# Kernel tuning notes

Measured on AMD Instinct MI355X. Metric: run time of the kernel, lower is better.

Reference implementation:

```python
import jax, jax.numpy as jnp
import numpy as np

B, N = 32, 4096
SA1 = (512, 0.2, 32)   # npoint, radius, nsample
SA2 = (128, 0.4, 64)
MLP1 = [3, 64, 64, 128]
MLP2 = [131, 128, 128, 256]   # 128 feats + 3 relative xyz
MLP3 = [259, 256, 512, 1024]  # 256 feats + 3 xyz (group_all)


def _mk_mlp(key, dims, prefix, d):
    for i in range(len(dims) - 1):
        key, k1 = jax.random.split(key)
        d[f"{prefix}_w{i}"] = jax.random.normal(k1, (dims[i], dims[i + 1]), jnp.float32) * (1.0 / np.sqrt(dims[i]))
        d[f"{prefix}_b{i}"] = jnp.zeros((dims[i + 1],), jnp.float32)
    return key


def setup_inputs() -> dict:
    key = jax.random.key(0)
    d = {}
    key, kx = jax.random.split(key)
    d["xyz"] = jax.random.uniform(kx, (B, N, 3), jnp.float32)  # normalized coords in [0,1)
    key = _mk_mlp(key, MLP1, "sa1", d)
    key = _mk_mlp(key, MLP2, "sa2", d)
    key = _mk_mlp(key, MLP3, "sa3", d)
    key, k1, k2 = jax.random.split(key, 3)
    d["cls_w"] = jax.random.normal(k1, (1024, 1), jnp.float32) * 0.03
    d["cls_b"] = jnp.zeros((1,), jnp.float32)
    d["reg_w"] = jax.random.normal(k2, (1024, 4), jnp.float32) * 0.03
    d["reg_b"] = jnp.zeros((4,), jnp.float32)
    return d


def fps(xyz, npoint):
    """Farthest point sampling. xyz: (B,N,3) -> idx (B,npoint) int32."""
    Bb, Nn, _ = xyz.shape

    def step(carry, _):
        dist, farthest = carry  # (B,N), (B,)
        centroid = jnp.take_along_axis(xyz, farthest[:, None, None], axis=1)  # (B,1,3)
        d = jnp.sum((xyz - centroid) ** 2, axis=-1)  # (B,N)
        dist = jnp.minimum(dist, d)
        nxt = jnp.argmax(dist, axis=-1).astype(jnp.int32)
        return (dist, nxt), farthest

    init = (jnp.full((Bb, Nn), 1e10, xyz.dtype), jnp.zeros((Bb,), jnp.int32))
    _, idx = jax.lax.scan(step, init, None, length=npoint)
    return idx.T  # (B,npoint)


def ball_query(radius, nsample, xyz, new_xyz):
    """xyz: (B,N,3), new_xyz: (B,S,3) -> idx (B,S,nsample) int32."""
    Bb, S, _ = new_xyz.shape
    Nn = xyz.shape[1]
    sqr = jnp.sum((new_xyz[:, :, None, :] - xyz[:, None, :, :]) ** 2, axis=-1)  # (B,S,N)
    idx = jnp.broadcast_to(jnp.arange(Nn, dtype=jnp.int32), (Bb, S, Nn))
    idx = jnp.where(sqr > radius * radius, Nn, idx)
    idx = jnp.sort(idx, axis=-1)[:, :, :nsample]
    first = idx[:, :, :1]
    return jnp.where(idx == Nn, first, idx)  # pad out-of-ball slots with first neighbor


def _sa(xyz, feats, npoint, radius, nsample, ws, bs):
    Bb = xyz.shape[0]
    cidx = fps(xyz, npoint)
    new_xyz = xyz[jnp.arange(Bb)[:, None], cidx]  # (B,S,3)
    gidx = ball_query(radius, nsample, xyz, new_xyz)  # (B,S,K)
    b3 = jnp.arange(Bb)[:, None, None]
    g = xyz[b3, gidx] - new_xyz[:, :, None, :]  # (B,S,K,3) relative coords
    if feats is not None:
        g = jnp.concatenate([g, feats[b3, gidx]], axis=-1)
    for w, b in zip(ws, bs):
        g = jax.nn.relu(g @ w + b)
    return new_xyz, jnp.max(g, axis=2)  # (B,S,C_out)


def _sa_all(xyz, feats, ws, bs):
    g = jnp.concatenate([xyz, feats], axis=-1)[:, None]  # (B,1,S,3+C)
    for w, b in zip(ws, bs):
        g = jax.nn.relu(g @ w + b)
    return jnp.max(g, axis=2)[:, 0]  # (B,C_out)


def reference(xyz, sa1_w0, sa1_b0, sa1_w1, sa1_b1, sa1_w2, sa1_b2,
              sa2_w0, sa2_b0, sa2_w1, sa2_b1, sa2_w2, sa2_b2,
              sa3_w0, sa3_b0, sa3_w1, sa3_b1, sa3_w2, sa3_b2,
              cls_w, cls_b, reg_w, reg_b):
    xyz1, f1 = _sa(xyz, None, SA1[0], SA1[1], SA1[2],
                   [sa1_w0, sa1_w1, sa1_w2], [sa1_b0, sa1_b1, sa1_b2])
    xyz2, f2 = _sa(xyz1, f1, SA2[0], SA2[1], SA2[2],
                   [sa2_w0, sa2_w1, sa2_w2], [sa2_b0, sa2_b1, sa2_b2])
    feat = _sa_all(xyz2, f2, [sa3_w0, sa3_w1, sa3_w2], [sa3_b0, sa3_b1, sa3_b2])  # (B,1024)
    return feat @ cls_w + cls_b, feat @ reg_w + reg_b
```

## Files before the change

kernel.cpp:

```cpp
#include <hip/hip_runtime.h>

#define DEVINL __device__ __forceinline__

typedef __attribute__((ext_vector_type(8))) short bf16x8;
typedef __attribute__((ext_vector_type(8))) unsigned short u16x8;
typedef __attribute__((ext_vector_type(4))) float f32x4;

DEVINL unsigned short f2bh(float f){
  unsigned u = __float_as_uint(f);
  return (unsigned short)((u + 0x7FFFu + ((u >> 16) & 1u)) >> 16);
}
DEVINL float bh2f(unsigned short h){ return __uint_as_float(((unsigned)h) << 16); }

DEVINL unsigned long long dpp_max_u64(unsigned long long k) {
#define DPP_STEP(ctrl)                                                        \
  {                                                                           \
    int hi = (int)(k >> 32), lo = (int)(unsigned)k;                           \
    int oh = __builtin_amdgcn_update_dpp(0, hi, ctrl, 0xF, 0xF, 1);           \
    int ol = __builtin_amdgcn_update_dpp(0, lo, ctrl, 0xF, 0xF, 1);           \
    unsigned long long ok =                                                   \
        ((unsigned long long)(unsigned)oh << 32) | (unsigned)ol;              \
    if (ok > k) k = ok;                                                       \
  }
  DPP_STEP(0x111)
  DPP_STEP(0x112)
  DPP_STEP(0x114)
  DPP_STEP(0x118)
  DPP_STEP(0x142)
  DPP_STEP(0x143)
#undef DPP_STEP
  return k;
}

template<int N, int NP, int NT>
DEVINL void fps_body(const float* __restrict__ xyz, float* __restrict__ nxyz,
                     int b, int t) {
  constexpr int PTS = N / NT;
  constexpr int NW = NT / 64;
  __shared__ float xs[N], ys[N], zs[N];
  __shared__ int farr[NP];
  __shared__ unsigned long long sk[2][(NW > 1 ? NW : 1)];
  float px[PTS], py[PTS], pz[PTS], dst[PTS];
  const float* base = xyz + (size_t)b * N * 3;
#pragma unroll
  for (int j = 0; j < PTS; ++j) {
    int i = t + j * NT;
    float x = base[i * 3 + 0], y = base[i * 3 + 1], z = base[i * 3 + 2];
    px[j] = x; py[j] = y; pz[j] = z;
    xs[i] = x; ys[i] = y; zs[i] = z;
    dst[j] = 1e10f;
  }
  __syncthreads();
  int far = 0;
  const int wv = t >> 6, ln = t & 63;
  for (int s = 0; s < NP; ++s) {
    float cx = xs[far], cy = ys[far], cz = zs[far];
    if (t == 0) farr[s] = far;
    float bv = -1.f; int bi = 0;
#pragma unroll
    for (int j = 0; j < PTS; ++j) {
      float dx = __fsub_rn(px[j], cx), dy = __fsub_rn(py[j], cy), dz = __fsub_rn(pz[j], cz);
      float d = __fadd_rn(__fadd_rn(__fmul_rn(dx, dx), __fmul_rn(dy, dy)), __fmul_rn(dz, dz));
      float nd = fminf(dst[j], d);
      dst[j] = nd;
      int i = t + j * NT;
      if (nd > bv) { bv = nd; bi = i; }
    }
    unsigned long long key =
        ((unsigned long long)__float_as_uint(bv) << 32) | (unsigned)(~bi);
    key = dpp_max_u64(key);
    if constexpr (NW == 1) {
      int rl = __builtin_amdgcn_readlane((int)(unsigned)key, 63);
      far = (int)(~(unsigned)rl);
    } else {
      const int p = s & 1;
      if (ln == 63) sk[p][wv] = key;
      __syncthreads();
      unsigned long long m = sk[p][0];
#pragma unroll
      for (int q = 1; q < NW; ++q) {
        unsigned long long qk = sk[p][q];
        if (qk > m) m = qk;
      }
      far = (int)(~(unsigned)m);
    }
  }
  __syncthreads();
  for (int s2 = t; s2 < NP; s2 += NT) {
    int fi = farr[s2];
    float* o = nxyz + ((size_t)b * NP + s2) * 3;
    o[0] = xs[fi]; o[1] = ys[fi]; o[2] = zs[fi];
  }
}

template<int N, int NS>
DEVINL void bq_body(const float* __restrict__ pts, const float* __restrict__ centers,
                    int* __restrict__ gidx, int Q, float r2, int blk, int t) {
  const int wv = t >> 6, ln = t & 63;
  const int g = blk * 4 + wv;
  const int b = g / Q, q = g % Q;
  const float* pb = pts + (size_t)b * N * 3;
  const float* c = centers + ((size_t)b * Q + q) * 3;
  const float cx = c[0], cy = c[1], cz = c[2];
  __shared__ int gbuf[4][NS];
  int taken = 0;
  for (int base = 0; base < N; base += 64) {
    if (taken >= NS) break;
    int i = base + ln;
    float dx = __fsub_rn(pb[i * 3 + 0], cx), dy = __fsub_rn(pb[i * 3 + 1], cy),
          dz = __fsub_rn(pb[i * 3 + 2], cz);
    float d = __fadd_rn(__fadd_rn(__fmul_rn(dx, dx), __fmul_rn(dy, dy)), __fmul_rn(dz, dz));
    bool in = (d <= r2);
    unsigned long long mk = __ballot(in);
    int rank = __popcll(mk & ((1ull << ln) - 1ull));
    int pos = taken + rank;
    if (in && pos < NS) gbuf[wv][pos] = i;
    taken += (int)__popcll(mk);
  }
  int total = taken < NS ? taken : NS;
  int first = gbuf[wv][0];
  int* out = gidx + ((size_t)b * Q + q) * NS;
  for (int j = ln; j < NS; j += 64) out[j] = (j < total) ? gbuf[wv][j] : first;
}

struct WPEnt { const float* W; unsigned short* hi; unsigned short* lo; int K, N, row0, beg, end; };
struct WPTab { WPEnt e[8]; };
DEVINL void wprep_body(const WPTab& tab, int idx) {
#pragma unroll
  for (int i = 0; i < 8; ++i) {
    const WPEnt& E = tab.e[i];
    if (idx >= E.beg && idx < E.end) {
      int local = idx - E.beg;
      int k = local / E.N, n = local - k * E.N;
      float v = E.W[(size_t)(E.row0 + k) * E.N + n];
      unsigned short h = f2bh(v);
      E.hi[(size_t)n * E.K + k] = h;
      E.lo[(size_t)n * E.K + k] = f2bh(v - bh2f(h));
    }
  }
}

__global__ __launch_bounds__(256) void fps1_wprep_kernel(const float* __restrict__ xyz,
                                                         float* __restrict__ nx1, WPTab tab) {
  if (blockIdx.x < 32) { fps_body<4096, 512, 256>(xyz, nx1, blockIdx.x, threadIdx.x); return; }
  wprep_body(tab, (blockIdx.x - 32) * 256 + threadIdx.x);
}

__global__ __launch_bounds__(256) void fps2_bq1_kernel(const float* __restrict__ xyz,
                                                       const float* __restrict__ nx1,
                                                       int* __restrict__ gidx1,
                                                       float* __restrict__ nx2, float r21) {
  if (blockIdx.x < 32) { fps_body<512, 128, 256>(nx1, nx2, blockIdx.x, threadIdx.x); return; }
  bq_body<4096, 32>(xyz, nx1, gidx1, 512, r21, blockIdx.x - 32, threadIdx.x);
}

template<int K, int N, int AS, int WS, bool XYZC>
DEVINL void do_layer(const unsigned short* __restrict__ Ghi, const unsigned short* __restrict__ Glo,
                     const float* __restrict__ Wxyz,
                     const float* __restrict__ A, unsigned short* __restrict__ Whi,
                     unsigned short* __restrict__ Wlo, const float* __restrict__ sxyz,
                     f32x4* acc, int t) {
  constexpr int KT = K / 32;
  constexpr int NCH = N / 64;
  constexpr int K8 = K / 8;
  constexpr int SI = (64 * K8) / 256;
  const int l = t & 63, wv = t >> 6;

  u16x8 rh[SI], rl[SI];
#pragma unroll
  for (int s = 0; s < SI; ++s) {
    int u = t + s * 256;
    int nn = u / K8, k8 = (u - nn * K8) * 8;
    rh[s] = *reinterpret_cast<const u16x8*>(Ghi + (size_t)nn * K + k8);
    rl[s] = *reinterpret_cast<const u16x8*>(Glo + (size_t)nn * K + k8);
  }

  bf16x8 ahi[KT], alo[KT];
  {
    const int row = wv * 16 + (l & 15);
    const float* ap = A + row * AS + (l >> 4) * 8;
#pragma unroll
    for (int kt = 0; kt < KT; ++kt) {
      float4 v0 = *reinterpret_cast<const float4*>(ap + kt * 32);
      float4 v1 = *reinterpret_cast<const float4*>(ap + kt * 32 + 4);
      float f[8] = {v0.x, v0.y, v0.z, v0.w, v1.x, v1.y, v1.z, v1.w};
      bf16x8 h, lo2;
#pragma unroll
      for (int j = 0; j < 8; ++j) {
        unsigned short hb = f2bh(f[j]);
        h[j] = (short)hb;
        lo2[j] = (short)f2bh(f[j] - bh2f(hb));
      }
      ahi[kt] = h; alo[kt] = lo2;
    }
  }
#pragma unroll
  for (int i = 0; i < N / 16; ++i) acc[i] = f32x4{0.f, 0.f, 0.f, 0.f};

#pragma unroll
  for (int c = 0; c < NCH; ++c) {
    __syncthreads();
#pragma unroll
    for (int s = 0; s < SI; ++s) {
      int u = t + s * 256;
      int nn = u / K8, k8 = (u - nn * K8) * 8;
      *reinterpret_cast<u16x8*>(Whi + nn * WS + k8) = rh[s];
      *reinterpret_cast<u16x8*>(Wlo + nn * WS + k8) = rl[s];
    }
    if (c + 1 < NCH) {
#pragma unroll
      for (int s = 0; s < SI; ++s) {
        int u = t + s * 256;
        int nn = u / K8, k8 = (u - nn * K8) * 8;
        rh[s] = *reinterpret_cast<const u16x8*>(Ghi + (size_t)((c + 1) * 64 + nn) * K + k8);
        rl[s] = *reinterpret_cast<const u16x8*>(Glo + (size_t)((c + 1) * 64 + nn) * K + k8);
      }
    }
    __syncthreads();
#pragma unroll
    for (int ct = 0; ct < 4; ++ct) {
      const unsigned short* wp = Whi + (ct * 16 + (l & 15)) * WS + (l >> 4) * 8;
      const unsigned short* wq = Wlo + (ct * 16 + (l & 15)) * WS + (l >> 4) * 8;
      f32x4 a = acc[c * 4 + ct];
#pragma unroll
      for (int kt = 0; kt < KT; ++kt) {
        bf16x8 wh = *reinterpret_cast<const bf16x8*>(wp + kt * 32);
        bf16x8 wl = *reinterpret_cast<const bf16x8*>(wq + kt * 32);
        a = __builtin_amdgcn_mfma_f32_16x16x32_bf16(ahi[kt], wh, a, 0, 0, 0);
        a = __builtin_amdgcn_mfma_f32_16x16x32_bf16(alo[kt], wh, a, 0, 0, 0);
        a = __builtin_amdgcn_mfma_f32_16x16x32_bf16(ahi[kt], wl, a, 0, 0, 0);
      }
      acc[c * 4 + ct] = a;
    }
  }
  if constexpr (XYZC) {
    float xr[4][3];
#pragma unroll
    for (int r = 0; r < 4; ++r) {
      int row = wv * 16 + (l >> 4) * 4 + r;
      xr[r][0] = sxyz[row * 4 + 0];
      xr[r][1] = sxyz[row * 4 + 1];
      xr[r][2] = sxyz[row * 4 + 2];
    }
#pragma unroll
    for (int gt = 0; gt < N / 16; ++gt) {
      int col = gt * 16 + (l & 15);
      float w0 = Wxyz[col], w1 = Wxyz[N + col], w2 = Wxyz[2 * N + col];
#pragma unroll
      for (int r = 0; r < 4; ++r)
        acc[gt][r] += xr[r][0] * w0 + xr[r][1] * w1 + xr[r][2] * w2;
    }
  }
}

template<int NPTS, int Q, int M, int GPB, int FD, int C1, int C2, int C3>
__global__ __launch_bounds__(256) void sa_mfma_kernel(
    const float* __restrict__ pts, const float* __restrict__ centers,
    const int* __restrict__ gidx, const float* __restrict__ feats,
    const float* __restrict__ W0, const float* __restrict__ B0,
    const unsigned short* __restrict__ G0h, const unsigned short* __restrict__ G0l,
    const unsigned short* __restrict__ G1h, const unsigned short* __restrict__ G1l,
    const float* __restrict__ B1,
    const unsigned short* __restrict__ G2h, const unsigned short* __restrict__ G2l,
    const float* __restrict__ B2,
    float* __restrict__ fout) {
  static_assert(M * GPB == 64, "");
  constexpr int MK1 = (FD > C1 ? FD : C1);
  constexpr int MAXK = (MK1 > C2 ? MK1 : C2);
  constexpr int AS = MAXK + 12;
  constexpr int WS = MAXK + 8;
  __shared__ __align__(16) float A[64 * AS];
  __shared__ __align__(16) unsigned short Whi[64 * WS];
  __shared__ __align__(16) unsigned short Wlo[64 * WS];
  __shared__ float sxyz[64 * 4];
  __shared__ int idxs[64];
  __shared__ float ctr[GPB][4];
  __shared__ float red[4][C3];

  const int t = threadIdx.x;
  const int blk = blockIdx.x;
  const int b = blk / (Q / GPB);
  const int q0 = (blk % (Q / GPB)) * GPB;
  const int l = t & 63, wv = t >> 6;

  if (t < GPB * 3) {
    int g = t / 3, c2 = t % 3;
    ctr[g][c2] = centers[((size_t)b * Q + q0 + g) * 3 + c2];
  }
  for (int m = t; m < 64; m += 256)
    idxs[m] = gidx[((size_t)b * Q + q0 + (m / M)) * M + (m % M)];
  __syncthreads();
  const float* pb = pts + (size_t)b * NPTS * 3;
  for (int m = t; m < 64; m += 256) {
    int g = m / M, i = idxs[m];
    sxyz[m * 4 + 0] = pb[i * 3 + 0] - ctr[g][0];
    sxyz[m * 4 + 1] = pb[i * 3 + 1] - ctr[g][1];
    sxyz[m * 4 + 2] = pb[i * 3 + 2] - ctr[g][2];
  }
  if constexpr (FD > 0) {
    const int m = t >> 2, co = (t & 3) * (FD / 4);
    const float* src = feats + ((size_t)b * NPTS + idxs[m]) * FD + co;
    float* dst = A + m * AS + co;
#pragma unroll
    for (int j = 0; j < FD / 4; j += 4)
      *reinterpret_cast<float4*>(dst + j) = *reinterpret_cast<const float4*>(src + j);
  }
  __syncthreads();

  f32x4 acc[C3 / 16];

  if constexpr (FD == 0) {
    for (int u = t; u < 64 * C1; u += 256) {
      int m = u / C1, c2 = u - m * C1;
      float v = B0[c2] + sxyz[m * 4 + 0] * W0[0 * C1 + c2]
                       + sxyz[m * 4 + 1] * W0[1 * C1 + c2]
                       + sxyz[m * 4 + 2] * W0[2 * C1 + c2];
      A[m * AS + c2] = fmaxf(v, 0.f);
    }
    __syncthreads();
  } else {
    do_layer<FD, C1, AS, WS, true>(G0h, G0l, W0, A, Whi, Wlo, sxyz, acc, t);
#pragma unroll
    for (int gt = 0; gt < C1 / 16; ++gt) {
      int col = gt * 16 + (l & 15);
      float bia = B0[col];
#pragma unroll
      for (int r = 0; r < 4; ++r)
        A[(wv * 16 + (l >> 4) * 4 + r) * AS + col] = fmaxf(acc[gt][r] + bia, 0.f);
    }
  }

  do_layer<C1, C2, AS, WS, false>(G1h, G1l, nullptr, A, Whi, Wlo, sxyz, acc, t);
#pragma unroll
  for (int gt = 0; gt < C2 / 16; ++gt) {
    int col = gt * 16 + (l & 15);
    float bia = B1[col];
#pragma unroll
    for (int r = 0; r < 4; ++r)
      A[(wv * 16 + (l >> 4) * 4 + r) * AS + col] = fmaxf(acc[gt][r] + bia, 0.f);
  }

  do_layer<C2, C3, AS, WS, false>(G2h, G2l, nullptr, A, Whi, Wlo, sxyz, acc, t);
#pragma unroll
  for (int gt = 0; gt < C3 / 16; ++gt) {
    int col = gt * 16 + (l & 15);
    float v = fmaxf(fmaxf(acc[gt][0], acc[gt][1]), fmaxf(acc[gt][2], acc[gt][3]));
    v = fmaxf(v, __shfl_xor(v, 16, 64));
    v = fmaxf(v, __shfl_xor(v, 32, 64));
    if (l < 16) red[wv][col] = v + B2[col];
  }
  __syncthreads();
  constexpr int WPG = 4 / GPB;
  for (int u = t; u < GPB * C3; u += 256) {
    int g = u / C3, c2 = u - g * C3;
    float v = red[g * WPG][c2];
#pragma unroll
    for (int w = 1; w < WPG; ++w) v = fmaxf(v, red[g * WPG + w][c2]);
    fout[((size_t)b * Q + q0 + g) * C3 + c2] = fmaxf(v, 0.f);
  }
}

template<int NPTS, int Q, int M, int GPB>
DEVINL void sa1_body(const float* __restrict__ pts, const float* __restrict__ centers,
                     const int* __restrict__ gidx,
                     const float* __restrict__ W0, const float* __restrict__ B0,
                     const unsigned short* __restrict__ G1h, const unsigned short* __restrict__ G1l,
                     const float* __restrict__ B1,
                     const unsigned short* __restrict__ G2h, const unsigned short* __restrict__ G2l,
                     const float* __restrict__ B2,
                     float* __restrict__ fout, int blk, int t) {
  static_assert(M * GPB == 64, "");
  constexpr int C1 = 64, C2 = 64, C3 = 128;
  constexpr int AS = 76;
  constexpr int WS = 72;
  constexpr int NC = C2 + C3;
  __shared__ __align__(16) float A[64 * AS];
  __shared__ __align__(16) unsigned short Wh[NC * WS];
  __shared__ __align__(16) unsigned short Wl[NC * WS];
  __shared__ float sxyz[64 * 4];
  __shared__ int idxs[64];
  __shared__ float ctr[GPB][4];
  __shared__ float red[4][C3];

  const int l = t & 63, wv = t >> 6;
  const int b = blk / (Q / GPB);
  const int q0 = (blk % (Q / GPB)) * GPB;

  if (t < GPB * 3) {
    int g = t / 3, c2 = t % 3;
    ctr[g][c2] = centers[((size_t)b * Q + q0 + g) * 3 + c2];
  }
  for (int m = t; m < 64; m += 256)
    idxs[m] = gidx[((size_t)b * Q + q0 + (m / M)) * M + (m % M)];
  for (int u = t; u < NC * 8; u += 256) {
    int col = u >> 3, k8 = (u & 7) * 8;
    const unsigned short* sh = (col < C2) ? G1h + (size_t)col * 64 + k8
                                          : G2h + (size_t)(col - C2) * 64 + k8;
    const unsigned short* sl = (col < C2) ? G1l + (size_t)col * 64 + k8
                                          : G2l + (size_t)(col - C2) * 64 + k8;
    *reinterpret_cast<u16x8*>(Wh + col * WS + k8) = *reinterpret_cast<const u16x8*>(sh);
    *reinterpret_cast<u16x8*>(Wl + col * WS + k8) = *reinterpret_cast<const u16x8*>(sl);
  }
  __syncthreads();
  const float* pb = pts + (size_t)b * NPTS * 3;
  for (int m = t; m < 64; m += 256) {
    int g = m / M, i = idxs[m];
    sxyz[m * 4 + 0] = pb[i * 3 + 0] - ctr[g][0];
    sxyz[m * 4 + 1] = pb[i * 3 + 1] - ctr[g][1];
    sxyz[m * 4 + 2] = pb[i * 3 + 2] - ctr[g][2];
  }
  __syncthreads();

  for (int u = t; u < 64 * C1; u += 256) {
    int m = u / C1, c2 = u - m * C1;
    float v = B0[c2] + sxyz[m * 4 + 0] * W0[0 * C1 + c2]
                     + sxyz[m * 4 + 1] * W0[1 * C1 + c2]
                     + sxyz[m * 4 + 2] * W0[2 * C1 + c2];
    A[m * AS + c2] = fmaxf(v, 0.f);
  }
  __syncthreads();

  f32x4 acc[8];
  {
    bf16x8 ah[2], al[2];
    const float* ap = A + (wv * 16 + (l & 15)) * AS + (l >> 4) * 8;
#pragma unroll
    for (int kt = 0; kt < 2; ++kt) {
      float4 v0 = *reinterpret_cast<const float4*>(ap + kt * 32);
      float4 v1 = *reinterpret_cast<const float4*>(ap + kt * 32 + 4);
      float f[8] = {v0.x, v0.y, v0.z, v0.w, v1.x, v1.y, v1.z, v1.w};
      bf16x8 h, lo2;
#pragma unroll
      for (int j = 0; j < 8; ++j) {
        unsigned short hb = f2bh(f[j]);
        h[j] = (short)hb;
        lo2[j] = (short)f2bh(f[j] - bh2f(hb));
      }
      ah[kt] = h; al[kt] = lo2;
    }
#pragma unroll
    for (int i = 0; i < 4; ++i) acc[i] = f32x4{0.f, 0.f, 0.f, 0.f};
#pragma unroll
    for (int ct = 0; ct < 4; ++ct) {
      const unsigned short* wp = Wh + (ct * 16 + (l & 15)) * WS + (l >> 4) * 8;
      const unsigned short* wq = Wl + (ct * 16 + (l & 15)) * WS + (l >> 4) * 8;
      f32x4 a = acc[ct];
#pragma unroll
      for (int kt = 0; kt < 2; ++kt) {
        bf16x8 wh = *reinterpret_cast<const bf16x8*>(wp + kt * 32);
        bf16x8 wl = *reinterpret_cast<const bf16x8*>(wq + kt * 32);
        a = __builtin_amdgcn_mfma_f32_16x16x32_bf16(ah[kt], wh, a, 0, 0, 0);
        a = __builtin_amdgcn_mfma_f32_16x16x32_bf16(al[kt], wh, a, 0, 0, 0);
        a = __builtin_amdgcn_mfma_f32_16x16x32_bf16(ah[kt], wl, a, 0, 0, 0);
      }
      acc[ct] = a;
    }
#pragma unroll
    for (int gt = 0; gt < 4; ++gt) {
      int col = gt * 16 + (l & 15);
      float bia = B1[col];
#pragma unroll
      for (int r = 0; r < 4; ++r)
        A[(wv * 16 + (l >> 4) * 4 + r) * AS + col] = fmaxf(acc[gt][r] + bia, 0.f);
    }
  }

  {
    bf16x8 ah[2], al[2];
    const float* ap = A + (wv * 16 + (l & 15)) * AS + (l >> 4) * 8;
#pragma unroll
    for (int kt = 0; kt < 2; ++kt) {
      float4 v0 = *reinterpret_cast<const float4*>(ap + kt * 32);
      float4 v1 = *reinterpret_cast<const float4*>(ap + kt * 32 + 4);
      float f[8] = {v0.x, v0.y, v0.z, v0.w, v1.x, v1.y, v1.z, v1.w};
      bf16x8 h, lo2;
#pragma unroll
      for (int j = 0; j < 8; ++j) {
        unsigned short hb = f2bh(f[j]);
        h[j] = (short)hb;
        lo2[j] = (short)f2bh(f[j] - bh2f(hb));
      }
      ah[kt] = h; al[kt] = lo2;
    }
#pragma unroll
    for (int i = 0; i < 8; ++i) acc[i] = f32x4{0.f, 0.f, 0.f, 0.f};
#pragma unroll
    for (int gt = 0; gt < 8; ++gt) {
      const unsigned short* wp = Wh + (C2 + gt * 16 + (l & 15)) * WS + (l >> 4) * 8;
      const unsigned short* wq = Wl + (C2 + gt * 16 + (l & 15)) * WS + (l >> 4) * 8;
      f32x4 a = acc[gt];
#pragma unroll
      for (int kt = 0; kt < 2; ++kt) {
        bf16x8 wh = *reinterpret_cast<const bf16x8*>(wp + kt * 32);
        bf16x8 wl = *reinterpret_cast<const bf16x8*>(wq + kt * 32);
        a = __builtin_amdgcn_mfma_f32_16x16x32_bf16(ah[kt], wh, a, 0, 0, 0);
        a = __builtin_amdgcn_mfma_f32_16x16x32_bf16(al[kt], wh, a, 0, 0, 0);
        a = __builtin_amdgcn_mfma_f32_16x16x32_bf16(ah[kt], wl, a, 0, 0, 0);
      }
      acc[gt] = a;
    }
#pragma unroll
    for (int gt = 0; gt < 8; ++gt) {
      int col = gt * 16 + (l & 15);
      float v = fmaxf(fmaxf(acc[gt][0], acc[gt][1]), fmaxf(acc[gt][2], acc[gt][3]));
      v = fmaxf(v, __shfl_xor(v, 16, 64));
      v = fmaxf(v, __shfl_xor(v, 32, 64));
      if (l < 16) red[wv][col] = v + B2[col];
    }
  }
  __syncthreads();
  constexpr int WPG = 4 / GPB;
  for (int u = t; u < GPB * C3; u += 256) {
    int g = u / C3, c2 = u - g * C3;
    float v = red[g * WPG][c2];
#pragma unroll
    for (int w = 1; w < WPG; ++w) v = fmaxf(v, red[g * WPG + w][c2]);
    fout[((size_t)b * Q + q0 + g) * C3 + c2] = fmaxf(v, 0.f);
  }
}

__global__ __launch_bounds__(256) void bq2_sa1_kernel(
    const float* __restrict__ xyz, const float* __restrict__ nx1,
    const float* __restrict__ nx2, int* __restrict__ gidx2, float r22,
    const int* __restrict__ gidx1,
    const float* __restrict__ s1w0, const float* __restrict__ s1b0,
    const unsigned short* __restrict__ g11h, const unsigned short* __restrict__ g11l,
    const float* __restrict__ s1b1,
    const unsigned short* __restrict__ g12h, const unsigned short* __restrict__ g12l,
    const float* __restrict__ s1b2, float* __restrict__ f1) {
  if (blockIdx.x < 1024) {
    bq_body<512, 64>(nx1, nx2, gidx2, 128, r22, blockIdx.x, threadIdx.x);
    return;
  }
  sa1_body<4096, 512, 32, 2>(xyz, nx1, gidx1, s1w0, s1b0, g11h, g11l, s1b1,
                             g12h, g12l, s1b2, f1, blockIdx.x - 1024, threadIdx.x);
}

constexpr int AS3 = 532;
DEVINL void sa3_frags(const float* __restrict__ A, int l, int KT, bf16x8* ahi, bf16x8* alo) {
  const float* ap = A + (l & 15) * AS3 + (l >> 4) * 8;
  for (int kt = 0; kt < KT; ++kt) {
    float4 v0 = *reinterpret_cast<const float4*>(ap + kt * 32);
    float4 v1 = *reinterpret_cast<const float4*>(ap + kt * 32 + 4);
    float f[8] = {v0.x, v0.y, v0.z, v0.w, v1.x, v1.y, v1.z, v1.w};
    bf16x8 h, lo2;
#pragma unroll
    for (int j = 0; j < 8; ++j) {
      unsigned short hb = f2bh(f[j]);
      h[j] = (short)hb;
      lo2[j] = (short)f2bh(f[j] - bh2f(hb));
    }
    ahi[kt] = h; alo[kt] = lo2;
  }
}

template<int K>
DEVINL void sa3_mm64(const unsigned short* __restrict__ Gh, const unsigned short* __restrict__ Gl,
                     int ncol0, int l, const bf16x8* ahi, const bf16x8* alo, f32x4* acc4) {
  constexpr int KT = K / 32;
#pragma unroll
  for (int ct = 0; ct < 4; ++ct) {
    const unsigned short* hp = Gh + (size_t)(ncol0 + ct * 16 + (l & 15)) * K + (l >> 4) * 8;
    const unsigned short* lp = Gl + (size_t)(ncol0 + ct * 16 + (l & 15)) * K + (l >> 4) * 8;
    f32x4 a = acc4[ct];
#pragma unroll
    for (int kt = 0; kt < KT; ++kt) {
      bf16x8 wh = *reinterpret_cast<const bf16x8*>(hp + kt * 32);
      bf16x8 wl = *reinterpret_cast<const bf16x8*>(lp + kt * 32);
      a = __builtin_amdgcn_mfma_f32_16x16x32_bf16(ahi[kt], wh, a, 0, 0, 0);
      a = __builtin_amdgcn_mfma_f32_16x16x32_bf16(alo[kt], wh, a, 0, 0, 0);
      a = __builtin_amdgcn_mfma_f32_16x16x32_bf16(ahi[kt], wl, a, 0, 0, 0);
    }
    acc4[ct] = a;
  }
}

__global__ __launch_bounds__(256) void sa3f_kernel(
    const float* __restrict__ nx2, const float* __restrict__ f2,
    const float* __restrict__ W0full,
    const unsigned short* __restrict__ G0h, const unsigned short* __restrict__ G0l,
    const float* __restrict__ B0,
    const unsigned short* __restrict__ G1h, const unsigned short* __restrict__ G1l,
    const float* __restrict__ B1,
    const unsigned short* __restrict__ G2h, const unsigned short* __restrict__ G2l,
    const float* __restrict__ B2,
    float* __restrict__ partial) {
  __shared__ __align__(16) float A[16 * AS3];
  __shared__ float sxyz[16][4];
  const int t = threadIdx.x, l = t & 63, w = t >> 6;
  const int b = blockIdx.x >> 3, rb = blockIdx.x & 7;
  const int row0 = rb * 16;
  {
    int r = t >> 4, cc = (t & 15) * 16;
    const float* src = f2 + ((size_t)b * 128 + row0 + r) * 256 + cc;
    float* dstp = A + r * AS3 + cc;
#pragma unroll
    for (int j = 0; j < 16; j += 4)
      *reinterpret_cast<float4*>(dstp + j) = *reinterpret_cast<const float4*>(src + j);
    if (t < 16) {
      const float* s = nx2 + ((size_t)b * 128 + row0 + t) * 3;
      sxyz[t][0] = s[0]; sxyz[t][1] = s[1]; sxyz[t][2] = s[2];
    }
  }
  __syncthreads();

  {
    bf16x8 ah[8], al[8];
    sa3_frags(A, l, 8, ah, al);
    __syncthreads();
    f32x4 acc[4];
#pragma unroll
    for (int i = 0; i < 4; ++i) acc[i] = f32x4{0.f, 0.f, 0.f, 0.f};
    sa3_mm64<256>(G0h, G0l, w * 64, l, ah, al, acc);
    float xr[4][3];
#pragma unroll
    for (int r = 0; r < 4; ++r) {
      int row = (l >> 4) * 4 + r;
      xr[r][0] = sxyz[row][0]; xr[r][1] = sxyz[row][1]; xr[r][2] = sxyz[row][2];
    }
#pragma unroll
    for (int ct = 0; ct < 4; ++ct) {
      int col = w * 64 + ct * 16 + (l & 15);
      float w0 = W0full[col], w1 = W0full[256 + col], w2 = W0full[512 + col];
      float bia = B0[col];
#pragma unroll
      for (int r = 0; r < 4; ++r) {
        int row = (l >> 4) * 4 + r;
        float v = acc[ct][r] + xr[r][0] * w0 + xr[r][1] * w1 + xr[r][2] * w2 + bia;
        A[row * AS3 + col] = fmaxf(v, 0.f);
      }
    }
    __syncthreads();
  }

  {
    bf16x8 ah[8], al[8];
    sa3_frags(A, l, 8, ah, al);
    __syncthreads();
    f32x4 acc[8];
#pragma unroll
    for (int i = 0; i < 8; ++i) acc[i] = f32x4{0.f, 0.f, 0.f, 0.f};
    sa3_mm64<256>(G1h, G1l, w * 128, l, ah, al, acc);
    sa3_mm64<256>(G1h, G1l, w * 128 + 64, l, ah, al, acc + 4);
#pragma unroll
    for (int cc = 0; cc < 8; ++cc) {
      int col = w * 128 + cc * 16 + (l & 15);
      float bia = B1[col];
#pragma unroll
      for (int r = 0; r < 4; ++r) {
        int row = (l >> 4) * 4 + r;
        A[row * AS3 + col] = fmaxf(acc[cc][r] + bia, 0.f);
      }
    }
    __syncthreads();
  }

  {
    bf16x8 ah[16], al[16];
    sa3_frags(A, l, 16, ah, al);
    float* pout = partial + ((size_t)(b * 8 + rb)) * 1024;
#pragma unroll
    for (int sub = 0; sub < 4; ++sub) {
      f32x4 acc[4];
#pragma unroll
      for (int i = 0; i < 4; ++i) acc[i] = f32x4{0.f, 0.f, 0.f, 0.f};
      sa3_mm64<512>(G2h, G2l, w * 256 + sub * 64, l, ah, al, acc);
#pragma unroll
      for (int ct = 0; ct < 4; ++ct) {
        int col = w * 256 + sub * 64 + ct * 16 + (l & 15);
        float v = fmaxf(fmaxf(acc[ct][0], acc[ct][1]), fmaxf(acc[ct][2], acc[ct][3]));
        v = fmaxf(v, __shfl_xor(v, 16, 64));
        v = fmaxf(v, __shfl_xor(v, 32, 64));
        if (l < 16) pout[col] = v + B2[col];
      }
    }
  }
}

__global__ __launch_bounds__(256) void heads_kernel(const float* __restrict__ partial,
                                                    const float* __restrict__ cw,
                                                    const float* __restrict__ cb,
                                                    const float* __restrict__ rw,
                                                    const float* __restrict__ rb,
                                                    float* __restrict__ out) {
  const int b = blockIdx.x, t = threadIdx.x;
  const float* pb = partial + (size_t)b * 8 * 1024;
  float a0 = 0, a1 = 0, a2 = 0, a3 = 0, a4 = 0;
  for (int k = t; k < 1024; k += 256) {
    float m = pb[k];
#pragma unroll
    for (int p = 1; p < 8; ++p) m = fmaxf(m, pb[p * 1024 + k]);
    float f = fmaxf(m, 0.f);
    a0 += f * cw[k];
    const float* r = rw + (size_t)k * 4;
    a1 += f * r[0]; a2 += f * r[1]; a3 += f * r[2]; a4 += f * r[3];
  }
#pragma unroll
  for (int m = 32; m >= 1; m >>= 1) {
    a0 += __shfl_xor(a0, m, 64); a1 += __shfl_xor(a1, m, 64);
    a2 += __shfl_xor(a2, m, 64); a3 += __shfl_xor(a3, m, 64);
    a4 += __shfl_xor(a4, m, 64);
  }
  __shared__ float red[4][5];
  const int wv = t >> 6, ln = t & 63;
  if (ln == 0) { red[wv][0] = a0; red[wv][1] = a1; red[wv][2] = a2; red[wv][3] = a3; red[wv][4] = a4; }
  __syncthreads();
  if (t == 0) {
    float s0 = red[0][0] + red[1][0] + red[2][0] + red[3][0];
    float s1 = red[0][1] + red[1][1] + red[2][1] + red[3][1];
    float s2 = red[0][2] + red[1][2] + red[2][2] + red[3][2];
    float s3 = red[0][3] + red[1][3] + red[2][3] + red[3][3];
    float s4 = red[0][4] + red[1][4] + red[2][4] + red[3][4];
    out[b] = s0 + cb[0];
    out[32 + b * 4 + 0] = s1 + rb[0];
    out[32 + b * 4 + 1] = s2 + rb[1];
    out[32 + b * 4 + 2] = s3 + rb[2];
    out[32 + b * 4 + 3] = s4 + rb[3];
  }
}

extern "C" void kernel_launch(void* const* d_in, const int* in_sizes, int n_in,
                              void* d_out, int out_size, void* d_ws, size_t ws_size,
                              hipStream_t stream) {
  (void)in_sizes; (void)n_in; (void)out_size; (void)ws_size;
  const float* xyz  = (const float*)d_in[0];
  const float* s1w0 = (const float*)d_in[1];  const float* s1b0 = (const float*)d_in[2];
  const float* s1w1 = (const float*)d_in[3];  const float* s1b1 = (const float*)d_in[4];
  const float* s1w2 = (const float*)d_in[5];  const float* s1b2 = (const float*)d_in[6];
  const float* s2w0 = (const float*)d_in[7];  const float* s2b0 = (const float*)d_in[8];
  const float* s2w1 = (const float*)d_in[9];  const float* s2b1 = (const float*)d_in[10];
  const float* s2w2 = (const float*)d_in[11]; const float* s2b2 = (const float*)d_in[12];
  const float* s3w0 = (const float*)d_in[13]; const float* s3b0 = (const float*)d_in[14];
  const float* s3w1 = (const float*)d_in[15]; const float* s3b1 = (const float*)d_in[16];
  const float* s3w2 = (const float*)d_in[17]; const float* s3b2 = (const float*)d_in[18];
  const float* clsw = (const float*)d_in[19]; const float* clsb = (const float*)d_in[20];
  const float* regw = (const float*)d_in[21]; const float* regb = (const float*)d_in[22];

  char* ws = (char*)d_ws;
  float* nx1   = (float*)(ws + 0);
  int*   gidx1 = (int*)  (ws + 196608);
  float* f1    = (float*)(ws + 2293760);
  float* nx2   = (float*)(ws + 10682368);
  int*   gidx2 = (int*)  (ws + 10731520);
  float* f2    = (float*)(ws + 11780096);

  unsigned short* wt = (unsigned short*)(ws + 20168704);
  unsigned short* g11h = wt;
  unsigned short* g11l = wt + 4096;
  unsigned short* g12h = wt + 8192;
  unsigned short* g12l = wt + 16384;
  unsigned short* g20h = wt + 24576;
  unsigned short* g20l = wt + 40960;
  unsigned short* g21h = wt + 57344;
  unsigned short* g21l = wt + 73728;
  unsigned short* g22h = wt + 90112;
  unsigned short* g22l = wt + 122880;
  unsigned short* g30h = (unsigned short*)(ws + 20480000);
  unsigned short* g30l = (unsigned short*)(ws + 20611072);
  unsigned short* g31h = (unsigned short*)(ws + 20742144);
  unsigned short* g31l = (unsigned short*)(ws + 21004288);
  unsigned short* g32h = (unsigned short*)(ws + 21266432);
  unsigned short* g32l = (unsigned short*)(ws + 22315008);
  float* partial = (float*)(ws + 23363584);

  const float r21 = (float)(0.2 * 0.2);
  const float r22 = (float)(0.4 * 0.4);

  WPTab tab;
  int off = 0;
  auto set = [&](int i, const float* W, unsigned short* hi, unsigned short* lo,
                 int K, int N, int row0) {
    tab.e[i] = WPEnt{W, hi, lo, K, N, row0, off, off + K * N};
    off += K * N;
  };
  set(0, s1w1, g11h, g11l, 64, 64, 0);
  set(1, s1w2, g12h, g12l, 64, 128, 0);
  set(2, s2w0, g20h, g20l, 128, 128, 3);
  set(3, s2w1, g21h, g21l, 128, 128, 0);
  set(4, s2w2, g22h, g22l, 128, 256, 0);
  set(5, s3w0, g30h, g30l, 256, 256, 3);
  set(6, s3w1, g31h, g31l, 256, 512, 0);
  set(7, s3w2, g32h, g32l, 512, 1024, 0);
  const int wblocks = (off + 255) / 256;

  fps1_wprep_kernel<<<32 + wblocks, 256, 0, stream>>>(xyz, nx1, tab);
  fps2_bq1_kernel<<<32 + 4096, 256, 0, stream>>>(xyz, nx1, gidx1, nx2, r21);
  bq2_sa1_kernel<<<1024 + 8192, 256, 0, stream>>>(
      xyz, nx1, nx2, gidx2, r22, gidx1,
      s1w0, s1b0, g11h, g11l, s1b1, g12h, g12l, s1b2, f1);
  sa_mfma_kernel<512, 128, 64, 1, 128, 128, 128, 256><<<4096, 256, 0, stream>>>(
      nx1, nx2, gidx2, f1, s2w0, s2b0,
      g20h, g20l, g21h, g21l, s2b1, g22h, g22l, s2b2, f2);
  sa3f_kernel<<<256, 256, 0, stream>>>(nx2, f2, s3w0, g30h, g30l, s3b0,
                                       g31h, g31l, s3b1, g32h, g32l, s3b2, partial);
  heads_kernel<<<32, 256, 0, stream>>>(partial, clsw, clsb, regw, regb, (float*)d_out);
}
```

Before: 728.4 us.

## Batch SA1 tiles per block, widen SA2 blocks, single-wave FPS2

Three changes. The SA1 body now loops over four tiles per block, so the bf16 weight split is staged into LDS once per block instead of once per tile, and the launch grid shrinks to match. The SA2 MLP kernel runs 512 threads on two query groups (128 rows) per block, so each LDS weight chunk is reused over twice the rows. The second FPS runs on a single wave (64 threads, 8 points each), which drops the cross-wave __syncthreads and LDS reduction from every sampling step. In exchange there is less block-level parallelism, more LDS per SA2 block (lower occupancy), and each FPS lane does more serial work.

```diff
diff --git a/kernel.cpp b/kernel.cpp
--- a/kernel.cpp
+++ b/kernel.cpp
@@ -50,7 +50,7 @@
     xs[i] = x; ys[i] = y; zs[i] = z;
     dst[j] = 1e10f;
   }
-  __syncthreads();
+  if constexpr (NW > 1) __syncthreads();
   int far = 0;
   const int wv = t >> 6, ln = t & 63;
   for (int s = 0; s < NP; ++s) {
@@ -85,7 +85,7 @@
       far = (int)(~(unsigned)m);
     }
   }
-  __syncthreads();
+  if constexpr (NW > 1) __syncthreads();
   for (int s2 = t; s2 < NP; s2 += NT) {
     int fi = farr[s2];
     float* o = nxyz + ((size_t)b * NP + s2) * 3;
@@ -150,11 +150,14 @@
                                                        const float* __restrict__ nx1,
                                                        int* __restrict__ gidx1,
                                                        float* __restrict__ nx2, float r21) {
-  if (blockIdx.x < 32) { fps_body<512, 128, 256>(nx1, nx2, blockIdx.x, threadIdx.x); return; }
+  if (blockIdx.x < 32) {
+    if (threadIdx.x < 64) fps_body<512, 128, 64>(nx1, nx2, blockIdx.x, threadIdx.x);
+    return;
+  }
   bq_body<4096, 32>(xyz, nx1, gidx1, 512, r21, blockIdx.x - 32, threadIdx.x);
 }
 
-template<int K, int N, int AS, int WS, bool XYZC>
+template<int K, int N, int AS, int WS, bool XYZC, int NTH>
 DEVINL void do_layer(const unsigned short* __restrict__ Ghi, const unsigned short* __restrict__ Glo,
                      const float* __restrict__ Wxyz,
                      const float* __restrict__ A, unsigned short* __restrict__ Whi,
@@ -163,13 +166,13 @@
   constexpr int KT = K / 32;
   constexpr int NCH = N / 64;
   constexpr int K8 = K / 8;
-  constexpr int SI = (64 * K8) / 256;
+  constexpr int SI = (64 * K8) / NTH;
   const int l = t & 63, wv = t >> 6;
 
   u16x8 rh[SI], rl[SI];
 #pragma unroll
   for (int s = 0; s < SI; ++s) {
-    int u = t + s * 256;
+    int u = t + s * NTH;
     int nn = u / K8, k8 = (u - nn * K8) * 8;
     rh[s] = *reinterpret_cast<const u16x8*>(Ghi + (size_t)nn * K + k8);
     rl[s] = *reinterpret_cast<const u16x8*>(Glo + (size_t)nn * K + k8);
@@ -202,7 +205,7 @@
     __syncthreads();
 #pragma unroll
     for (int s = 0; s < SI; ++s) {
-      int u = t + s * 256;
+      int u = t + s * NTH;
       int nn = u / K8, k8 = (u - nn * K8) * 8;
       *reinterpret_cast<u16x8*>(Whi + nn * WS + k8) = rh[s];
       *reinterpret_cast<u16x8*>(Wlo + nn * WS + k8) = rl[s];
@@ -210,7 +213,7 @@
     if (c + 1 < NCH) {
 #pragma unroll
       for (int s = 0; s < SI; ++s) {
-        int u = t + s * 256;
+        int u = t + s * NTH;
         int nn = u / K8, k8 = (u - nn * K8) * 8;
         rh[s] = *reinterpret_cast<const u16x8*>(Ghi + (size_t)((c + 1) * 64 + nn) * K + k8);
         rl[s] = *reinterpret_cast<const u16x8*>(Glo + (size_t)((c + 1) * 64 + nn) * K + k8);
@@ -254,7 +257,7 @@
 }
 
 template<int NPTS, int Q, int M, int GPB, int FD, int C1, int C2, int C3>
-__global__ __launch_bounds__(256) void sa_mfma_kernel(
+__global__ __launch_bounds__(512) void sa2_kernel(
     const float* __restrict__ pts, const float* __restrict__ centers,
     const int* __restrict__ gidx, const float* __restrict__ feats,
     const float* __restrict__ W0, const float* __restrict__ B0,
@@ -264,18 +267,21 @@
     const unsigned short* __restrict__ G2h, const unsigned short* __restrict__ G2l,
     const float* __restrict__ B2,
     float* __restrict__ fout) {
-  static_assert(M * GPB == 64, "");
+  constexpr int NTH = 512;
+  constexpr int ROWS = M * GPB;
+  constexpr int NWV = NTH / 64;
+  static_assert(ROWS == 16 * NWV, "wave owns 16 rows");
   constexpr int MK1 = (FD > C1 ? FD : C1);
   constexpr int MAXK = (MK1 > C2 ? MK1 : C2);
   constexpr int AS = MAXK + 12;
   constexpr int WS = MAXK + 8;
-  __shared__ __align__(16) float A[64 * AS];
+  __shared__ __align__(16) float A[ROWS * AS];
   __shared__ __align__(16) unsigned short Whi[64 * WS];
   __shared__ __align__(16) unsigned short Wlo[64 * WS];
-  __shared__ float sxyz[64 * 4];
-  __shared__ int idxs[64];
+  __shared__ float sxyz[ROWS * 4];
+  __shared__ int idxs[ROWS];
   __shared__ float ctr[GPB][4];
-  __shared__ float red[4][C3];
+  __shared__ float red[NWV][C3];
 
   const int t = threadIdx.x;
   const int blk = blockIdx.x;
@@ -287,17 +293,17 @@
     int g = t / 3, c2 = t % 3;
     ctr[g][c2] = centers[((size_t)b * Q + q0 + g) * 3 + c2];
   }
-  for (int m = t; m < 64; m += 256)
+  for (int m = t; m < ROWS; m += NTH)
     idxs[m] = gidx[((size_t)b * Q + q0 + (m / M)) * M + (m % M)];
   __syncthreads();
   const float* pb = pts + (size_t)b * NPTS * 3;
-  for (int m = t; m < 64; m += 256) {
+  for (int m = t; m < ROWS; m += NTH) {
     int g = m / M, i = idxs[m];
     sxyz[m * 4 + 0] = pb[i * 3 + 0] - ctr[g][0];
     sxyz[m * 4 + 1] = pb[i * 3 + 1] - ctr[g][1];
     sxyz[m * 4 + 2] = pb[i * 3 + 2] - ctr[g][2];
   }
-  if constexpr (FD > 0) {
+  {
     const int m = t >> 2, co = (t & 3) * (FD / 4);
     const float* src = feats + ((size_t)b * NPTS + idxs[m]) * FD + co;
     float* dst = A + m * AS + co;
@@ -309,28 +315,17 @@
 
   f32x4 acc[C3 / 16];
 
-  if constexpr (FD == 0) {
-    for (int u = t; u < 64 * C1; u += 256) {
-      int m = u / C1, c2 = u - m * C1;
-      float v = B0[c2] + sxyz[m * 4 + 0] * W0[0 * C1 + c2]
-                       + sxyz[m * 4 + 1] * W0[1 * C1 + c2]
-                       + sxyz[m * 4 + 2] * W0[2 * C1 + c2];
-      A[m * AS + c2] = fmaxf(v, 0.f);
-    }
-    __syncthreads();
-  } else {
-    do_layer<FD, C1, AS, WS, true>(G0h, G0l, W0, A, Whi, Wlo, sxyz, acc, t);
-#pragma unroll
-    for (int gt = 0; gt < C1 / 16; ++gt) {
-      int col = gt * 16 + (l & 15);
-      float bia = B0[col];
-#pragma unroll
-      for (int r = 0; r < 4; ++r)
-        A[(wv * 16 + (l >> 4) * 4 + r) * AS + col] = fmaxf(acc[gt][r] + bia, 0.f);
-    }
-  }
-
-  do_layer<C1, C2, AS, WS, false>(G1h, G1l, nullptr, A, Whi, Wlo, sxyz, acc, t);
+  do_layer<FD, C1, AS, WS, true, NTH>(G0h, G0l, W0, A, Whi, Wlo, sxyz, acc, t);
+#pragma unroll
+  for (int gt = 0; gt < C1 / 16; ++gt) {
+    int col = gt * 16 + (l & 15);
+    float bia = B0[col];
+#pragma unroll
+    for (int r = 0; r < 4; ++r)
+      A[(wv * 16 + (l >> 4) * 4 + r) * AS + col] = fmaxf(acc[gt][r] + bia, 0.f);
+  }
+
+  do_layer<C1, C2, AS, WS, false, NTH>(G1h, G1l, nullptr, A, Whi, Wlo, sxyz, acc, t);
 #pragma unroll
   for (int gt = 0; gt < C2 / 16; ++gt) {
     int col = gt * 16 + (l & 15);
@@ -340,7 +335,7 @@
       A[(wv * 16 + (l >> 4) * 4 + r) * AS + col] = fmaxf(acc[gt][r] + bia, 0.f);
   }
 
-  do_layer<C2, C3, AS, WS, false>(G2h, G2l, nullptr, A, Whi, Wlo, sxyz, acc, t);
+  do_layer<C2, C3, AS, WS, false, NTH>(G2h, G2l, nullptr, A, Whi, Wlo, sxyz, acc, t);
 #pragma unroll
   for (int gt = 0; gt < C3 / 16; ++gt) {
     int col = gt * 16 + (l & 15);
@@ -350,8 +345,8 @@
     if (l < 16) red[wv][col] = v + B2[col];
   }
   __syncthreads();
-  constexpr int WPG = 4 / GPB;
-  for (int u = t; u < GPB * C3; u += 256) {
+  constexpr int WPG = NWV / GPB;
+  for (int u = t; u < GPB * C3; u += NTH) {
     int g = u / C3, c2 = u - g * C3;
     float v = red[g * WPG][c2];
 #pragma unroll
@@ -360,7 +355,7 @@
   }
 }
 
-template<int NPTS, int Q, int M, int GPB>
+template<int NPTS, int Q, int M, int GPB, int TPB>
 DEVINL void sa1_body(const float* __restrict__ pts, const float* __restrict__ centers,
                      const int* __restrict__ gidx,
                      const float* __restrict__ W0, const float* __restrict__ B0,
@@ -368,7 +363,7 @@
                      const float* __restrict__ B1,
                      const unsigned short* __restrict__ G2h, const unsigned short* __restrict__ G2l,
                      const float* __restrict__ B2,
-                     float* __restrict__ fout, int blk, int t) {
+                     float* __restrict__ fout, int sblk, int t) {
   static_assert(M * GPB == 64, "");
   constexpr int C1 = 64, C2 = 64, C3 = 128;
   constexpr int AS = 76;
@@ -383,15 +378,7 @@
   __shared__ float red[4][C3];
 
   const int l = t & 63, wv = t >> 6;
-  const int b = blk / (Q / GPB);
-  const int q0 = (blk % (Q / GPB)) * GPB;
-
-  if (t < GPB * 3) {
-    int g = t / 3, c2 = t % 3;
-    ctr[g][c2] = centers[((size_t)b * Q + q0 + g) * 3 + c2];
-  }
-  for (int m = t; m < 64; m += 256)
-    idxs[m] = gidx[((size_t)b * Q + q0 + (m / M)) * M + (m % M)];
+
   for (int u = t; u < NC * 8; u += 256) {
     int col = u >> 3, k8 = (u & 7) * 8;
     const unsigned short* sh = (col < C2) ? G1h + (size_t)col * 64 + k8
@@ -401,121 +388,135 @@
     *reinterpret_cast<u16x8*>(Wh + col * WS + k8) = *reinterpret_cast<const u16x8*>(sh);
     *reinterpret_cast<u16x8*>(Wl + col * WS + k8) = *reinterpret_cast<const u16x8*>(sl);
   }
-  __syncthreads();
-  const float* pb = pts + (size_t)b * NPTS * 3;
-  for (int m = t; m < 64; m += 256) {
-    int g = m / M, i = idxs[m];
-    sxyz[m * 4 + 0] = pb[i * 3 + 0] - ctr[g][0];
-    sxyz[m * 4 + 1] = pb[i * 3 + 1] - ctr[g][1];
-    sxyz[m * 4 + 2] = pb[i * 3 + 2] - ctr[g][2];
-  }
-  __syncthreads();
-
-  for (int u = t; u < 64 * C1; u += 256) {
-    int m = u / C1, c2 = u - m * C1;
-    float v = B0[c2] + sxyz[m * 4 + 0] * W0[0 * C1 + c2]
-                     + sxyz[m * 4 + 1] * W0[1 * C1 + c2]
-                     + sxyz[m * 4 + 2] * W0[2 * C1 + c2];
-    A[m * AS + c2] = fmaxf(v, 0.f);
-  }
-  __syncthreads();
-
-  f32x4 acc[8];
-  {
-    bf16x8 ah[2], al[2];
-    const float* ap = A + (wv * 16 + (l & 15)) * AS + (l >> 4) * 8;
-#pragma unroll
-    for (int kt = 0; kt < 2; ++kt) {
-      float4 v0 = *reinterpret_cast<const float4*>(ap + kt * 32);
-      float4 v1 = *reinterpret_cast<const float4*>(ap + kt * 32 + 4);
-      float f[8] = {v0.x, v0.y, v0.z, v0.w, v1.x, v1.y, v1.z, v1.w};
-      bf16x8 h, lo2;
-#pragma unroll
-      for (int j = 0; j < 8; ++j) {
-        unsigned short hb = f2bh(f[j]);
-        h[j] = (short)hb;
-        lo2[j] = (short)f2bh(f[j] - bh2f(hb));
-      }
-      ah[kt] = h; al[kt] = lo2;
-    }
-#pragma unroll
-    for (int i = 0; i < 4; ++i) acc[i] = f32x4{0.f, 0.f, 0.f, 0.f};
-#pragma unroll
-    for (int ct = 0; ct < 4; ++ct) {
-      const unsigned short* wp = Wh + (ct * 16 + (l & 15)) * WS + (l >> 4) * 8;
-      const unsigned short* wq = Wl + (ct * 16 + (l & 15)) * WS + (l >> 4) * 8;
-      f32x4 a = acc[ct];
+
+  for (int it = 0; it < TPB; ++it) {
+    const int blk = sblk * TPB + it;
+    const int b = blk / (Q / GPB);
+    const int q0 = (blk % (Q / GPB)) * GPB;
+
+    if (t < GPB * 3) {
+      int g = t / 3, c2 = t % 3;
+      ctr[g][c2] = centers[((size_t)b * Q + q0 + g) * 3 + c2];
+    }
+    for (int m = t; m < 64; m += 256)
+      idxs[m] = gidx[((size_t)b * Q + q0 + (m / M)) * M + (m % M)];
+    __syncthreads();
+    const float* pb = pts + (size_t)b * NPTS * 3;
+    for (int m = t; m < 64; m += 256) {
+      int g = m / M, i = idxs[m];
+      sxyz[m * 4 + 0] = pb[i * 3 + 0] - ctr[g][0];
+      sxyz[m * 4 + 1] = pb[i * 3 + 1] - ctr[g][1];
+      sxyz[m * 4 + 2] = pb[i * 3 + 2] - ctr[g][2];
+    }
+    __syncthreads();
+
+    for (int u = t; u < 64 * C1; u += 256) {
+      int m = u / C1, c2 = u - m * C1;
+      float v = B0[c2] + sxyz[m * 4 + 0] * W0[0 * C1 + c2]
+                       + sxyz[m * 4 + 1] * W0[1 * C1 + c2]
+                       + sxyz[m * 4 + 2] * W0[2 * C1 + c2];
+      A[m * AS + c2] = fmaxf(v, 0.f);
+    }
+    __syncthreads();
+
+    f32x4 acc[8];
+    {
+      bf16x8 ah[2], al[2];
+      const float* ap = A + (wv * 16 + (l & 15)) * AS + (l >> 4) * 8;
 #pragma unroll
       for (int kt = 0; kt < 2; ++kt) {
-        bf16x8 wh = *reinterpret_cast<const bf16x8*>(wp + kt * 32);
-        bf16x8 wl = *reinterpret_cast<const bf16x8*>(wq + kt * 32);
-        a = __builtin_amdgcn_mfma_f32_16x16x32_bf16(ah[kt], wh, a, 0, 0, 0);
-        a = __builtin_amdgcn_mfma_f32_16x16x32_bf16(al[kt], wh, a, 0, 0, 0);
-        a = __builtin_amdgcn_mfma_f32_16x16x32_bf16(ah[kt], wl, a, 0, 0, 0);
-      }
-      acc[ct] = a;
-    }
-#pragma unroll
-    for (int gt = 0; gt < 4; ++gt) {
-      int col = gt * 16 + (l & 15);
-      float bia = B1[col];
-#pragma unroll
-      for (int r = 0; r < 4; ++r)
-        A[(wv * 16 + (l >> 4) * 4 + r) * AS + col] = fmaxf(acc[gt][r] + bia, 0.f);
-    }
-  }
-
-  {
-    bf16x8 ah[2], al[2];
-    const float* ap = A + (wv * 16 + (l & 15)) * AS + (l >> 4) * 8;
-#pragma unroll
-    for (int kt = 0; kt < 2; ++kt) {
-      float4 v0 = *reinterpret_cast<const float4*>(ap + kt * 32);
-      float4 v1 = *reinterpret_cast<const float4*>(ap + kt * 32 + 4);
-      float f[8] = {v0.x, v0.y, v0.z, v0.w, v1.x, v1.y, v1.z, v1.w};
-      bf16x8 h, lo2;
-#pragma unroll
-      for (int j = 0; j < 8; ++j) {
-        unsigned short hb = f2bh(f[j]);
-        h[j] = (short)hb;
-        lo2[j] = (short)f2bh(f[j] - bh2f(hb));
-      }
-      ah[kt] = h; al[kt] = lo2;
-    }
-#pragma unroll
-    for (int i = 0; i < 8; ++i) acc[i] = f32x4{0.f, 0.f, 0.f, 0.f};
-#pragma unroll
-    for (int gt = 0; gt < 8; ++gt) {
-      const unsigned short* wp = Wh + (C2 + gt * 16 + (l & 15)) * WS + (l >> 4) * 8;
-      const unsigned short* wq = Wl + (C2 + gt * 16 + (l & 15)) * WS + (l >> 4) * 8;
-      f32x4 a = acc[gt];
+        float4 v0 = *reinterpret_cast<const float4*>(ap + kt * 32);
+        float4 v1 = *reinterpret_cast<const float4*>(ap + kt * 32 + 4);
+        float f[8] = {v0.x, v0.y, v0.z, v0.w, v1.x, v1.y, v1.z, v1.w};
+        bf16x8 h, lo2;
+#pragma unroll
+        for (int j = 0; j < 8; ++j) {
+          unsigned short hb = f2bh(f[j]);
+          h[j] = (short)hb;
+          lo2[j] = (short)f2bh(f[j] - bh2f(hb));
+        }
+        ah[kt] = h; al[kt] = lo2;
+      }
+#pragma unroll
+      for (int i = 0; i < 4; ++i) acc[i] = f32x4{0.f, 0.f, 0.f, 0.f};
+#pragma unroll
+      for (int ct = 0; ct < 4; ++ct) {
+        const unsigned short* wp = Wh + (ct * 16 + (l & 15)) * WS + (l >> 4) * 8;
+        const unsigned short* wq = Wl + (ct * 16 + (l & 15)) * WS + (l >> 4) * 8;
+        f32x4 a = acc[ct];
+#pragma unroll
+        for (int kt = 0; kt < 2; ++kt) {
+          bf16x8 wh = *reinterpret_cast<const bf16x8*>(wp + kt * 32);
+          bf16x8 wl = *reinterpret_cast<const bf16x8*>(wq + kt * 32);
+          a = __builtin_amdgcn_mfma_f32_16x16x32_bf16(ah[kt], wh, a, 0, 0, 0);
+          a = __builtin_amdgcn_mfma_f32_16x16x32_bf16(al[kt], wh, a, 0, 0, 0);
+          a = __builtin_amdgcn_mfma_f32_16x16x32_bf16(ah[kt], wl, a, 0, 0, 0);
+        }
+        acc[ct] = a;
+      }
+#pragma unroll
+      for (int gt = 0; gt < 4; ++gt) {
+        int col = gt * 16 + (l & 15);
+        float bia = B1[col];
+#pragma unroll
+        for (int r = 0; r < 4; ++r)
+          A[(wv * 16 + (l >> 4) * 4 + r) * AS + col] = fmaxf(acc[gt][r] + bia, 0.f);
+      }
+    }
+
+    {
+      bf16x8 ah[2], al[2];
+      const float* ap = A + (wv * 16 + (l & 15)) * AS + (l >> 4) * 8;
 #pragma unroll
       for (int kt = 0; kt < 2; ++kt) {
-        bf16x8 wh = *reinterpret_cast<const bf16x8*>(wp + kt * 32);
-        bf16x8 wl = *reinterpret_cast<const bf16x8*>(wq + kt * 32);
-        a = __builtin_amdgcn_mfma_f32_16x16x32_bf16(ah[kt], wh, a, 0, 0, 0);
-        a = __builtin_amdgcn_mfma_f32_16x16x32_bf16(al[kt], wh, a, 0, 0, 0);
-        a = __builtin_amdgcn_mfma_f32_16x16x32_bf16(ah[kt], wl, a, 0, 0, 0);
-      }
-      acc[gt] = a;
-    }
-#pragma unroll
-    for (int gt = 0; gt < 8; ++gt) {
-      int col = gt * 16 + (l & 15);
-      float v = fmaxf(fmaxf(acc[gt][0], acc[gt][1]), fmaxf(acc[gt][2], acc[gt][3]));
-      v = fmaxf(v, __shfl_xor(v, 16, 64));
-      v = fmaxf(v, __shfl_xor(v, 32, 64));
-      if (l < 16) red[wv][col] = v + B2[col];
-    }
-  }
-  __syncthreads();
-  constexpr int WPG = 4 / GPB;
-  for (int u = t; u < GPB * C3; u += 256) {
-    int g = u / C3, c2 = u - g * C3;
-    float v = red[g * WPG][c2];
-#pragma unroll
-    for (int w = 1; w < WPG; ++w) v = fmaxf(v, red[g * WPG + w][c2]);
-    fout[((size_t)b * Q + q0 + g) * C3 + c2] = fmaxf(v, 0.f);
+        float4 v0 = *reinterpret_cast<const float4*>(ap + kt * 32);
+        float4 v1 = *reinterpret_cast<const float4*>(ap + kt * 32 + 4);
+        float f[8] = {v0.x, v0.y, v0.z, v0.w, v1.x, v1.y, v1.z, v1.w};
+        bf16x8 h, lo2;
+#pragma unroll
+        for (int j = 0; j < 8; ++j) {
+          unsigned short hb = f2bh(f[j]);
+          h[j] = (short)hb;
+          lo2[j] = (short)f2bh(f[j] - bh2f(hb));
+        }
+        ah[kt] = h; al[kt] = lo2;
+      }
+#pragma unroll
+      for (int i = 0; i < 8; ++i) acc[i] = f32x4{0.f, 0.f, 0.f, 0.f};
+#pragma unroll
+      for (int gt = 0; gt < 8; ++gt) {
+        const unsigned short* wp = Wh + (C2 + gt * 16 + (l & 15)) * WS + (l >> 4) * 8;
+        const unsigned short* wq = Wl + (C2 + gt * 16 + (l & 15)) * WS + (l >> 4) * 8;
+        f32x4 a = acc[gt];
+#pragma unroll
+        for (int kt = 0; kt < 2; ++kt) {
+          bf16x8 wh = *reinterpret_cast<const bf16x8*>(wp + kt * 32);
+          bf16x8 wl = *reinterpret_cast<const bf16x8*>(wq + kt * 32);
+          a = __builtin_amdgcn_mfma_f32_16x16x32_bf16(ah[kt], wh, a, 0, 0, 0);
+          a = __builtin_amdgcn_mfma_f32_16x16x32_bf16(al[kt], wh, a, 0, 0, 0);
+          a = __builtin_amdgcn_mfma_f32_16x16x32_bf16(ah[kt], wl, a, 0, 0, 0);
+        }
+        acc[gt] = a;
+      }
+#pragma unroll
+      for (int gt = 0; gt < 8; ++gt) {
+        int col = gt * 16 + (l & 15);
+        float v = fmaxf(fmaxf(acc[gt][0], acc[gt][1]), fmaxf(acc[gt][2], acc[gt][3]));
+        v = fmaxf(v, __shfl_xor(v, 16, 64));
+        v = fmaxf(v, __shfl_xor(v, 32, 64));
+        if (l < 16) red[wv][col] = v + B2[col];
+      }
+    }
+    __syncthreads();
+    constexpr int WPG = 4 / GPB;
+    for (int u = t; u < GPB * C3; u += 256) {
+      int g = u / C3, c2 = u - g * C3;
+      float v = red[g * WPG][c2];
+#pragma unroll
+      for (int w = 1; w < WPG; ++w) v = fmaxf(v, red[g * WPG + w][c2]);
+      fout[((size_t)b * Q + q0 + g) * C3 + c2] = fmaxf(v, 0.f);
+    }
+    __syncthreads();
   }
 }
 
@@ -532,8 +533,8 @@
     bq_body<512, 64>(nx1, nx2, gidx2, 128, r22, blockIdx.x, threadIdx.x);
     return;
   }
-  sa1_body<4096, 512, 32, 2>(xyz, nx1, gidx1, s1w0, s1b0, g11h, g11l, s1b1,
-                             g12h, g12l, s1b2, f1, blockIdx.x - 1024, threadIdx.x);
+  sa1_body<4096, 512, 32, 2, 4>(xyz, nx1, gidx1, s1w0, s1b0, g11h, g11l, s1b1,
+                                g12h, g12l, s1b2, f1, blockIdx.x - 1024, threadIdx.x);
 }
 
 constexpr int AS3 = 532;
@@ -785,10 +786,10 @@
 
   fps1_wprep_kernel<<<32 + wblocks, 256, 0, stream>>>(xyz, nx1, tab);
   fps2_bq1_kernel<<<32 + 4096, 256, 0, stream>>>(xyz, nx1, gidx1, nx2, r21);
-  bq2_sa1_kernel<<<1024 + 8192, 256, 0, stream>>>(
+  bq2_sa1_kernel<<<1024 + 2048, 256, 0, stream>>>(
       xyz, nx1, nx2, gidx2, r22, gidx1,
       s1w0, s1b0, g11h, g11l, s1b1, g12h, g12l, s1b2, f1);
-  sa_mfma_kernel<512, 128, 64, 1, 128, 128, 128, 256><<<4096, 256, 0, stream>>>(
+  sa2_kernel<512, 128, 64, 2, 128, 128, 128, 256><<<2048, 512, 0, stream>>>(
       nx1, nx2, gidx2, f1, s2w0, s2b0,
       g20h, g20l, g21h, g21l, s2b1, g22h, g22l, s2b2, f2);
   sa3f_kernel<<<256, 256, 0, stream>>>(nx2, f2, s3w0, g30h, g30l, s3b0,
```

Measured after the change: 712.4 us. 1.02x faster.
